# Optimization experiments

Hardware: AMD Instinct MI355X
Metric: run time of the kernel (lower is better)

The kernel has to match this reference:

```python
import jax, jax.numpy as jnp
import numpy as np

EPS = 1e-5
K = 20
THRESH = 0.5

def _bn_relu(x, g, b, m, v):
    # eval-mode BatchNorm1d followed by ReLU
    return jax.nn.relu(g * (x - m) * jax.lax.rsqrt(v + EPS) + b)

def setup_inputs() -> dict:
    key = jax.random.key(0)
    ks = jax.random.split(key, 16)
    T, C, CI, E, NC = 16384, 256, 8, 5, 13
    B, N = 2, T // 2
    inp = {
        "f_sem": jax.random.normal(ks[0], (T, C), jnp.float32),
        "f_ins": jax.random.normal(ks[1], (T, CI), jnp.float32),
        # equal-size, sorted batch assignment (2 clouds of 8192 points)
        "batch": jnp.repeat(jnp.arange(B, dtype=jnp.int64), N),
        # semantic_adaptation_fc: Linear(C,C) + BN + ReLU
        "W_sem": jax.random.normal(ks[2], (C, C), jnp.float32) * (1.0 / np.sqrt(C)),
        "b_sem": jnp.zeros((C,), jnp.float32),
        "g_sem": jnp.ones((C,), jnp.float32),
        "beta_sem": jnp.zeros((C,), jnp.float32),
        "m_sem": jax.random.normal(ks[3], (C,), jnp.float32) * 0.1,
        "v_sem": jax.random.uniform(ks[4], (C,), jnp.float32, 0.5, 1.5),
        # inst_fc: Linear(8,C) + BN + ReLU
        "W_ins": jax.random.normal(ks[5], (CI, C), jnp.float32) * (1.0 / np.sqrt(CI)),
        "b_ins": jnp.zeros((C,), jnp.float32),
        "g_ins": jnp.ones((C,), jnp.float32),
        "beta_ins": jnp.zeros((C,), jnp.float32),
        "m_ins": jax.random.normal(ks[6], (C,), jnp.float32) * 0.1,
        "v_ins": jax.random.uniform(ks[7], (C,), jnp.float32, 0.5, 1.5),
        # instance_embedding_fc: plain Linear(C,E)
        "W_emb": jax.random.normal(ks[8], (C, E), jnp.float32) * (1.0 / np.sqrt(C)),
        "b_emb": jnp.zeros((E,), jnp.float32),
        # classifier_fc: plain Linear(C,NC)
        "W_cls": jax.random.normal(ks[9], (C, NC), jnp.float32) * (1.0 / np.sqrt(C)),
        "b_cls": jnp.zeros((NC,), jnp.float32),
    }
    return inp

def _instance_fusion(e_ins, f_sem, batch):
    # assumes sorted batch with equal-size segments (enforced by setup_inputs)
    T, C = f_sem.shape
    B = int(batch[-1]) + 1
    N = T // B
    e = e_ins.reshape(B, N, -1)
    f = f_sem.reshape(B, N, C)
    # squared Euclidean pairwise distances per cloud: [B, N, N]
    sq = jnp.sum(e * e, axis=-1)
    d2 = sq[:, :, None] + sq[:, None, :] - 2.0 * jnp.einsum("bnd,bmd->bnm", e, e)
    d2 = jnp.maximum(d2, 0.0)
    neg_vals, idx = jax.lax.top_k(-d2, K)          # k smallest distances, [B,N,K]
    within = (-neg_vals) <= THRESH * THRESH        # distance <= threshold
    self_idx = jnp.broadcast_to(jnp.arange(N)[None, :, None], idx.shape)
    col = jnp.where(within, idx, self_idx)         # fall back to self outside threshold
    neigh = jax.vmap(lambda fb, cb: fb[cb])(f, col)  # [B,N,K,C]
    return jnp.max(neigh, axis=2).reshape(T, C)      # scatter-max == max over neighbors

def reference(f_sem, f_ins, batch,
              W_sem, b_sem, g_sem, beta_sem, m_sem, v_sem,
              W_ins, b_ins, g_ins, beta_ins, m_ins, v_ins,
              W_emb, b_emb, W_cls, b_cls):
    f_sem_prime = _bn_relu(f_sem @ W_sem + b_sem, g_sem, beta_sem, m_sem, v_sem)
    f_ins_h = _bn_relu(f_ins @ W_ins + b_ins, g_ins, beta_ins, m_ins, v_ins)
    f_sins = f_ins_h + f_sem_prime
    e_ins = f_sins @ W_emb + b_emb
    f_isem = _instance_fusion(e_ins, f_sem, batch)
    p_sem = f_isem @ W_cls + b_cls
    return (p_sem, e_ins)
```

## Files before the change

### kernel.cpp

```cpp
#include <hip/hip_runtime.h>
#include <math.h>

#define T 16384
#define C 256
#define CI 8
#define EDIM 5
#define NC 13
#define NPTS 8192
#define KNN 20
#define CAP 256
#define FR 32
#define FRPB 8

typedef float f4v __attribute__((ext_vector_type(4)));
typedef _Float16 h8 __attribute__((ext_vector_type(8)));
typedef _Float16 h4v __attribute__((ext_vector_type(4)));

__global__ __launch_bounds__(256) void cvt_kernel(
    const float* __restrict__ f_sem, _Float16* __restrict__ fsem_h)
{
    const size_t i = (size_t)(blockIdx.x * 256 + threadIdx.x) * 8;
    const float4 a = *(const float4*)(f_sem + i);
    const float4 b = *(const float4*)(f_sem + i + 4);
    h8 h;
    h[0] = (_Float16)a.x; h[1] = (_Float16)a.y;
    h[2] = (_Float16)a.z; h[3] = (_Float16)a.w;
    h[4] = (_Float16)b.x; h[5] = (_Float16)b.y;
    h[6] = (_Float16)b.z; h[7] = (_Float16)b.w;
    *(h8*)(fsem_h + i) = h;
}

__global__ __launch_bounds__(256) void front_kernel(
    const float* __restrict__ f_sem, const float* __restrict__ f_ins,
    const float* __restrict__ W_sem, const float* __restrict__ b_sem,
    const float* __restrict__ g_sem, const float* __restrict__ beta_sem,
    const float* __restrict__ m_sem, const float* __restrict__ v_sem,
    const float* __restrict__ W_ins, const float* __restrict__ b_ins,
    const float* __restrict__ g_ins, const float* __restrict__ beta_ins,
    const float* __restrict__ m_ins, const float* __restrict__ v_ins,
    const float* __restrict__ W_emb, const float* __restrict__ b_emb,
    float* __restrict__ eA, double* __restrict__ eD,
    float* __restrict__ out_e)
{
    __shared__ __align__(16) _Float16 sAh[FR][264];
    __shared__ __align__(16) _Float16 sAl[FR][264];
    __shared__ float bnA1[C], bnB1[C], bnA2[C], bnB2[C];
    __shared__ float weL[C][EDIM];
    __shared__ float lfi[FR][CI];
    __shared__ float sP[4][FR][EDIM];

    const int tid = threadIdx.x;
    const int rowBase = blockIdx.x * FR;

    #pragma unroll
    for (int i = 0; i < 8; i++) {
        const int idx = tid + 256 * i;
        const int g = idx * 4;
        const int row = g >> 8, k = g & 255;
        const float4 v = *(const float4*)(f_sem + (size_t)rowBase * C + g);
        const float vv[4] = {v.x, v.y, v.z, v.w};
        #pragma unroll
        for (int q = 0; q < 4; q++) {
            const _Float16 h = (_Float16)vv[q];
            sAh[row][k + q] = h;
            sAl[row][k + q] = (_Float16)(vv[q] - (float)h);
        }
    }
    {
        const int c = tid;
        const float rs1 = 1.0f / sqrtf(v_sem[c] + 1e-5f);
        const float A1 = g_sem[c] * rs1;
        bnA1[c] = A1;
        bnB1[c] = A1 * (b_sem[c] - m_sem[c]) + beta_sem[c];
        const float rs2 = 1.0f / sqrtf(v_ins[c] + 1e-5f);
        const float A2 = g_ins[c] * rs2;
        bnA2[c] = A2;
        bnB2[c] = A2 * (b_ins[c] - m_ins[c]) + beta_ins[c];
        #pragma unroll
        for (int j = 0; j < EDIM; j++) weL[c][j] = W_emb[c * EDIM + j];
    }
    if (tid < FR * CI) lfi[tid >> 3][tid & 7] = f_ins[rowBase * CI + tid];
    __syncthreads();

    const int w = tid >> 6, lane = tid & 63;
    const int r16 = lane & 15, kq = lane >> 4;
    const int n0 = 64 * w;

    f4v acc[2][4];
    #pragma unroll
    for (int mi = 0; mi < 2; mi++)
        #pragma unroll
        for (int ni = 0; ni < 4; ni++) acc[mi][ni] = (f4v){0.f, 0.f, 0.f, 0.f};

    for (int kt = 0; kt < 8; kt++) {
        const int koff = 32 * kt + 8 * kq;
        const h8 ah0 = *(const h8*)&sAh[r16][koff];
        const h8 ah1 = *(const h8*)&sAh[r16 + 16][koff];
        const h8 al0 = *(const h8*)&sAl[r16][koff];
        const h8 al1 = *(const h8*)&sAl[r16 + 16][koff];
        #pragma unroll
        for (int ni = 0; ni < 4; ni++) {
            const float* wp = W_sem + (size_t)koff * C + (n0 + 16 * ni + r16);
            float wf[8];
            #pragma unroll
            for (int j = 0; j < 8; j++) wf[j] = wp[(size_t)j * C];
            h8 bh, bl;
            #pragma unroll
            for (int j = 0; j < 8; j++) {
                const _Float16 h = (_Float16)wf[j];
                bh[j] = h;
                bl[j] = (_Float16)(wf[j] - (float)h);
            }
            acc[0][ni] = __builtin_amdgcn_mfma_f32_16x16x32_f16(ah0, bh, acc[0][ni], 0, 0, 0);
            acc[1][ni] = __builtin_amdgcn_mfma_f32_16x16x32_f16(ah1, bh, acc[1][ni], 0, 0, 0);
            acc[0][ni] = __builtin_amdgcn_mfma_f32_16x16x32_f16(al0, bh, acc[0][ni], 0, 0, 0);
            acc[1][ni] = __builtin_amdgcn_mfma_f32_16x16x32_f16(al1, bh, acc[1][ni], 0, 0, 0);
            acc[0][ni] = __builtin_amdgcn_mfma_f32_16x16x32_f16(ah0, bl, acc[0][ni], 0, 0, 0);
            acc[1][ni] = __builtin_amdgcn_mfma_f32_16x16x32_f16(ah1, bl, acc[1][ni], 0, 0, 0);
        }
    }

    f4v prow, pcol;
    {
        const f4v z = {0.f, 0.f, 0.f, 0.f};
        h8 ra, rb, ca, cb;
        #pragma unroll
        for (int j = 0; j < 8; j++) {
            ra[j] = (_Float16)(float)r16;
            rb[j] = (_Float16)((kq == 0 && j == 0) ? 1.0f : 0.0f);
            ca[j] = rb[j];
            cb[j] = ra[j];
        }
        prow = __builtin_amdgcn_mfma_f32_16x16x32_f16(ra, rb, z, 0, 0, 0);
        pcol = __builtin_amdgcn_mfma_f32_16x16x32_f16(ca, cb, z, 0, 0, 0);
    }
    const int colm = (int)pcol[0];
    int rloc[4];
    #pragma unroll
    for (int r = 0; r < 4; r++) rloc[r] = (int)prow[r];

    float p[2][4][EDIM];
    #pragma unroll
    for (int mi = 0; mi < 2; mi++)
        #pragma unroll
        for (int r = 0; r < 4; r++)
            #pragma unroll
            for (int j = 0; j < EDIM; j++) p[mi][r][j] = 0.f;

    #pragma unroll
    for (int ni = 0; ni < 4; ni++) {
        const int c = n0 + 16 * ni + colm;
        const float A1 = bnA1[c], B1 = bnB1[c];
        const float A2 = bnA2[c], B2 = bnB2[c];
        float wi[CI], we[EDIM];
        #pragma unroll
        for (int k = 0; k < CI; k++) wi[k] = W_ins[k * C + c];
        #pragma unroll
        for (int j = 0; j < EDIM; j++) we[j] = weL[c][j];
        #pragma unroll
        for (int mi = 0; mi < 2; mi++)
            #pragma unroll
            for (int r = 0; r < 4; r++) {
                const int row = 16 * mi + rloc[r];
                float x2 = 0.f;
                #pragma unroll
                for (int k = 0; k < CI; k++) x2 = fmaf(lfi[row][k], wi[k], x2);
                const float h1 = fmaxf(fmaf(A1, acc[mi][ni][r], B1), 0.f);
                const float h2 = fmaxf(fmaf(A2, x2, B2), 0.f);
                const float s = h1 + h2;
                #pragma unroll
                for (int j = 0; j < EDIM; j++) p[mi][r][j] = fmaf(s, we[j], p[mi][r][j]);
            }
    }

    #pragma unroll
    for (int off = 1; off < 16; off <<= 1)
        #pragma unroll
        for (int mi = 0; mi < 2; mi++)
            #pragma unroll
            for (int r = 0; r < 4; r++)
                #pragma unroll
                for (int j = 0; j < EDIM; j++)
                    p[mi][r][j] += __shfl_xor(p[mi][r][j], off);

    if (r16 == 0) {
        #pragma unroll
        for (int mi = 0; mi < 2; mi++)
            #pragma unroll
            for (int r = 0; r < 4; r++)
                #pragma unroll
                for (int j = 0; j < EDIM; j++)
                    sP[w][16 * mi + rloc[r]][j] = p[mi][r][j];
    }
    __syncthreads();

    if (tid < FR) {
        const int row = rowBase + tid;
        double sq = 0.0;
        #pragma unroll
        for (int j = 0; j < EDIM; j++) {
            const float s = ((sP[0][tid][j] + sP[1][tid][j]) +
                             (sP[2][tid][j] + sP[3][tid][j])) + b_emb[j];
            const double ed = (double)s;
            eD[(size_t)row * 8 + j] = ed;
            sq = fma(ed, ed, sq);
            eA[(size_t)row * 8 + j] = s;
            out_e[(size_t)row * EDIM + j] = s;
        }
        eD[(size_t)row * 8 + 5] = sq;
        eA[(size_t)row * 8 + 5] = (float)sq;
        eA[(size_t)row * 8 + 6] = 0.f;
        eA[(size_t)row * 8 + 7] = 0.f;
    }
}

__device__ __attribute__((noinline)) float4 rescan_topk(
    const float* __restrict__ eA, const float* __restrict__ f_sem,
    const float* __restrict__ reRow, int cbase, int lane)
{
    float re0 = reRow[0], re1 = reRow[1], re2 = reRow[2];
    float re3 = reRow[3], re4 = reRow[4], sqF = reRow[5];
    float4 mx = make_float4(-3.4e38f, -3.4e38f, -3.4e38f, -3.4e38f);
    long long last = -1;
    for (int sel = 0; sel < KNN; sel++) {
        long long best = 0x7fffffffffffffffLL;
        for (int cb = 0; cb < NPTS; cb += 64) {
            const int j = cbase + cb + lane;
            const float4 ea = *(const float4*)(eA + (size_t)j * 8);
            const float2 eb = *(const float2*)(eA + (size_t)j * 8 + 4);
            float dot = re0 * ea.x;
            dot = fmaf(re1, ea.y, dot); dot = fmaf(re2, ea.z, dot);
            dot = fmaf(re3, ea.w, dot); dot = fmaf(re4, eb.x, dot);
            const float d2 = fmaxf((sqF + eb.y) - 2.f * dot, 0.f);
            long long key = (((long long)__float_as_uint(d2)) << 32)
                            | (unsigned int)(cb + lane);
            if (key <= last) key = 0x7fffffffffffffffLL;
            if (key < best) best = key;
        }
        #pragma unroll
        for (int off = 32; off; off >>= 1) {
            const long long o = __shfl_xor(best, off);
            if (o < best) best = o;
        }
        last = best;
        const int idx = (int)(best & 0xffffffffLL);
        const float4 fv = *(const float4*)(f_sem + (size_t)(cbase + idx) * C + lane * 4);
        mx.x = fmaxf(mx.x, fv.x); mx.y = fmaxf(mx.y, fv.y);
        mx.z = fmaxf(mx.z, fv.z); mx.w = fmaxf(mx.w, fv.w);
    }
    return mx;
}

template <bool H16>
__global__ __launch_bounds__(256) void knn_kernel(
    const float* __restrict__ eA, const double* __restrict__ eD,
    const float* __restrict__ f_sem, const _Float16* __restrict__ fsem_h,
    const float* __restrict__ W_cls, const float* __restrict__ b_cls,
    float* __restrict__ out_p)
{
    __shared__ float rA[FRPB][8];
    __shared__ double rD[FRPB][6];
    __shared__ unsigned short cidx[FRPB][CAP];
    __shared__ unsigned long long kP[FRPB][CAP];
    __shared__ int cntS[FRPB];
    __shared__ unsigned short memL[FRPB][24];
    __shared__ int nlS[FRPB];

    const int tid = threadIdx.x;
    const int rowBase = blockIdx.x * FRPB;

    if (tid < FRPB * 8) rA[tid >> 3][tid & 7] = eA[(rowBase + (tid >> 3)) * 8 + (tid & 7)];
    if (tid < FRPB * 6) rD[tid / 6][tid % 6] = eD[(rowBase + tid / 6) * 8 + tid % 6];
    if (tid < FRPB) cntS[tid] = 0;
    __syncthreads();

    const int wave = tid >> 6, lane = tid & 63;
    const int cbase = (rowBase >= NPTS) ? NPTS : 0;

    {
        float re[FRPB][5], thrb[FRPB];
        #pragma unroll
        for (int r = 0; r < FRPB; r++) {
            #pragma unroll
            for (int q = 0; q < 5; q++) re[r][q] = rA[r][q];
            thrb[r] = (rA[r][5] - 0.251f) * 0.5f;
        }

        const int cstart = wave * (NPTS / 4);
        for (int cb = cstart; cb < cstart + NPTS / 4; cb += 128) {
            const int j0 = cbase + cb + lane;
            const float4 ea0 = *(const float4*)(eA + (size_t)j0 * 8);
            const float2 eb0 = *(const float2*)(eA + (size_t)j0 * 8 + 4);
            const float4 ea1 = *(const float4*)(eA + (size_t)(j0 + 64) * 8);
            const float2 eb1 = *(const float2*)(eA + (size_t)(j0 + 64) * 8 + 4);
            const float hs0 = 0.5f * eb0.y, hs1 = 0.5f * eb1.y;
            #pragma unroll
            for (int r = 0; r < FRPB; r++) {
                float dot = re[r][0] * ea0.x;
                dot = fmaf(re[r][1], ea0.y, dot); dot = fmaf(re[r][2], ea0.z, dot);
                dot = fmaf(re[r][3], ea0.w, dot); dot = fmaf(re[r][4], eb0.x, dot);
                const bool rec = dot >= (thrb[r] + hs0);
                const unsigned long long m = __ballot(rec);
                if (m) {
                    int base;
                    if (lane == 0) base = atomicAdd(&cntS[r], (int)__popcll(m));
                    base = __shfl(base, 0);
                    const int pre = __builtin_amdgcn_mbcnt_hi(
                        (unsigned int)(m >> 32),
                        __builtin_amdgcn_mbcnt_lo((unsigned int)m, 0u));
                    const int pos = base + pre;
                    if (rec && pos < CAP) cidx[r][pos] = (unsigned short)(cb + lane);
                }
            }
            #pragma unroll
            for (int r = 0; r < FRPB; r++) {
                float dot = re[r][0] * ea1.x;
                dot = fmaf(re[r][1], ea1.y, dot); dot = fmaf(re[r][2], ea1.z, dot);
                dot = fmaf(re[r][3], ea1.w, dot); dot = fmaf(re[r][4], eb1.x, dot);
                const bool rec = dot >= (thrb[r] + hs1);
                const unsigned long long m = __ballot(rec);
                if (m) {
                    int base;
                    if (lane == 0) base = atomicAdd(&cntS[r], (int)__popcll(m));
                    base = __shfl(base, 0);
                    const int pre = __builtin_amdgcn_mbcnt_hi(
                        (unsigned int)(m >> 32),
                        __builtin_amdgcn_mbcnt_lo((unsigned int)m, 0u));
                    const int pos = base + pre;
                    if (rec && pos < CAP) cidx[r][pos] = (unsigned short)(cb + 64 + lane);
                }
            }
        }
    }
    __syncthreads();

    const int lr0 = 2 * wave, lr1 = lr0 + 1;

    #pragma unroll 1
    for (int rr = 0; rr < 2; rr++) {
        const int lr = lr0 + rr;
        const int cnt = cntS[lr];
        const double* rd = rD[lr];

        if (cnt <= CAP) {
            unsigned long long mykp[4];
            int myid[4], mpos[4];
            bool mem[4];
            #pragma unroll
            for (int q = 0; q < 4; q++) {
                const int i = lane + 64 * q;
                mykp[q] = ~0ull; myid[q] = -1; mem[q] = false;
                if (i < cnt) {
                    const int id = (int)cidx[lr][i];
                    const double* ep = eD + (size_t)(cbase + id) * 8;
                    double dotd = 0.0;
                    #pragma unroll
                    for (int qq = 0; qq < 5; qq++) dotd = fma(rd[qq], ep[qq], dotd);
                    const double d2 = fmax((rd[5] + ep[5]) - 2.0 * dotd, 0.0);
                    if (d2 <= 0.25) {
                        mem[q] = true;
                        const unsigned int k32 = __float_as_uint((float)d2);
                        mykp[q] = (((unsigned long long)k32) << 16) | (unsigned int)id;
                        myid[q] = id;
                    }
                }
            }
            int base = 0;
            #pragma unroll
            for (int q = 0; q < 4; q++) {
                const unsigned long long b = __ballot(mem[q]);
                if (mem[q]) {
                    const int pos = base + (int)__builtin_amdgcn_mbcnt_hi(
                        (unsigned int)(b >> 32),
                        __builtin_amdgcn_mbcnt_lo((unsigned int)b, 0u));
                    mpos[q] = pos;
                    kP[lr][pos] = mykp[q];
                }
                base += (int)__popcll(b);
            }
            const int m = base;

            if (m <= KNN) {
                #pragma unroll
                for (int q = 0; q < 4; q++)
                    if (mem[q]) memL[lr][mpos[q]] = (unsigned short)myid[q];
                if (lane == 0) nlS[lr] = m;
            } else {
                int rank[4] = {0, 0, 0, 0};
                for (int j = 0; j < m; j++) {
                    const unsigned long long kj = kP[lr][j];
                    #pragma unroll
                    for (int q = 0; q < 4; q++) rank[q] += (kj < mykp[q]) ? 1 : 0;
                }
                int sbase = 0;
                #pragma unroll
                for (int q = 0; q < 4; q++) {
                    const bool sel = mem[q] && (rank[q] < KNN);
                    const unsigned long long b = __ballot(sel);
                    if (sel) {
                        const int pos = sbase + (int)__builtin_amdgcn_mbcnt_hi(
                            (unsigned int)(b >> 32),
                            __builtin_amdgcn_mbcnt_lo((unsigned int)b, 0u));
                        memL[lr][pos] = (unsigned short)myid[q];
                    }
                    sbase += (int)__popcll(b);
                }
                if (lane == 0) nlS[lr] = sbase;
            }
        } else {
            if (lane == 0) { memL[lr][0] = 0; nlS[lr] = -1; }
        }
    }

    const int s0 = nlS[lr0], s1 = nlS[lr1];
    const bool fb0 = (s0 < 0), fb1 = (s1 < 0);
    const int n0 = fb0 ? 1 : s0, n1 = fb1 ? 1 : s1;
    float4 mx0 = make_float4(-3.4e38f, -3.4e38f, -3.4e38f, -3.4e38f);
    float4 mx1 = mx0;
    const int nmax = (n0 > n1) ? n0 : n1;

    if (H16) {
        for (int k = 0; k < nmax; k += 8) {
            int a[8], c[8];
            #pragma unroll
            for (int i = 0; i < 8; i++) {
                a[i] = (int)memL[lr0][(k + i < n0) ? k + i : n0 - 1];
                c[i] = (int)memL[lr1][(k + i < n1) ? k + i : n1 - 1];
            }
            h4v fa[8], fc[8];
            #pragma unroll
            for (int i = 0; i < 8; i++) {
                fa[i] = *(const h4v*)(fsem_h + (size_t)(cbase + a[i]) * C + lane * 4);
                fc[i] = *(const h4v*)(fsem_h + (size_t)(cbase + c[i]) * C + lane * 4);
            }
            #pragma unroll
            for (int i = 0; i < 8; i++) {
                mx0.x = fmaxf(mx0.x, (float)fa[i][0]);
                mx0.y = fmaxf(mx0.y, (float)fa[i][1]);
                mx0.z = fmaxf(mx0.z, (float)fa[i][2]);
                mx0.w = fmaxf(mx0.w, (float)fa[i][3]);
                mx1.x = fmaxf(mx1.x, (float)fc[i][0]);
                mx1.y = fmaxf(mx1.y, (float)fc[i][1]);
                mx1.z = fmaxf(mx1.z, (float)fc[i][2]);
                mx1.w = fmaxf(mx1.w, (float)fc[i][3]);
            }
        }
    } else {
        for (int k = 0; k < nmax; k += 4) {
            const int a0 = (int)memL[lr0][(k     < n0) ? k     : n0 - 1];
            const int a1 = (int)memL[lr0][(k + 1 < n0) ? k + 1 : n0 - 1];
            const int a2 = (int)memL[lr0][(k + 2 < n0) ? k + 2 : n0 - 1];
            const int a3 = (int)memL[lr0][(k + 3 < n0) ? k + 3 : n0 - 1];
            const int c0 = (int)memL[lr1][(k     < n1) ? k     : n1 - 1];
            const int c1 = (int)memL[lr1][(k + 1 < n1) ? k + 1 : n1 - 1];
            const int c2 = (int)memL[lr1][(k + 2 < n1) ? k + 2 : n1 - 1];
            const int c3 = (int)memL[lr1][(k + 3 < n1) ? k + 3 : n1 - 1];
            const float4 f0 = *(const float4*)(f_sem + (size_t)(cbase + a0) * C + lane * 4);
            const float4 f1 = *(const float4*)(f_sem + (size_t)(cbase + a1) * C + lane * 4);
            const float4 f2 = *(const float4*)(f_sem + (size_t)(cbase + a2) * C + lane * 4);
            const float4 f3 = *(const float4*)(f_sem + (size_t)(cbase + a3) * C + lane * 4);
            const float4 g0 = *(const float4*)(f_sem + (size_t)(cbase + c0) * C + lane * 4);
            const float4 g1 = *(const float4*)(f_sem + (size_t)(cbase + c1) * C + lane * 4);
            const float4 g2 = *(const float4*)(f_sem + (size_t)(cbase + c2) * C + lane * 4);
            const float4 g3 = *(const float4*)(f_sem + (size_t)(cbase + c3) * C + lane * 4);
            mx0.x = fmaxf(fmaxf(fmaxf(mx0.x, f0.x), fmaxf(f1.x, f2.x)), f3.x);
            mx0.y = fmaxf(fmaxf(fmaxf(mx0.y, f0.y), fmaxf(f1.y, f2.y)), f3.y);
            mx0.z = fmaxf(fmaxf(fmaxf(mx0.z, f0.z), fmaxf(f1.z, f2.z)), f3.z);
            mx0.w = fmaxf(fmaxf(fmaxf(mx0.w, f0.w), fmaxf(f1.w, f2.w)), f3.w);
            mx1.x = fmaxf(fmaxf(fmaxf(mx1.x, g0.x), fmaxf(g1.x, g2.x)), g3.x);
            mx1.y = fmaxf(fmaxf(fmaxf(mx1.y, g0.y), fmaxf(g1.y, g2.y)), g3.y);
            mx1.z = fmaxf(fmaxf(fmaxf(mx1.z, g0.z), fmaxf(g1.z, g2.z)), g3.z);
            mx1.w = fmaxf(fmaxf(fmaxf(mx1.w, g0.w), fmaxf(g1.w, g2.w)), g3.w);
        }
    }
    if (fb0) mx0 = rescan_topk(eA, f_sem, rA[lr0], cbase, lane);
    if (fb1) mx1 = rescan_topk(eA, f_sem, rA[lr1], cbase, lane);

    #pragma unroll 1
    for (int rr = 0; rr < 2; rr++) {
        const float4 mx = rr ? mx1 : mx0;
        float p[NC];
        #pragma unroll
        for (int k = 0; k < NC; k++) p[k] = 0.f;
        const float* w0 = W_cls + (4 * lane + 0) * NC;
        const float* w1 = W_cls + (4 * lane + 1) * NC;
        const float* w2 = W_cls + (4 * lane + 2) * NC;
        const float* w3 = W_cls + (4 * lane + 3) * NC;
        #pragma unroll
        for (int k = 0; k < NC; k++)
            p[k] = fmaf(mx.x, w0[k], fmaf(mx.y, w1[k], fmaf(mx.z, w2[k], fmaf(mx.w, w3[k], p[k]))));
        #pragma unroll
        for (int off = 32; off; off >>= 1)
            #pragma unroll
            for (int k = 0; k < NC; k++) p[k] += __shfl_xor(p[k], off);
        if (lane == 0) {
            const int row = rowBase + lr0 + rr;
            #pragma unroll
            for (int k = 0; k < NC; k++) out_p[row * NC + k] = p[k] + b_cls[k];
        }
    }
}

extern "C" void kernel_launch(void* const* d_in, const int* in_sizes, int n_in,
                              void* d_out, int out_size, void* d_ws, size_t ws_size,
                              hipStream_t stream) {
    (void)in_sizes; (void)n_in; (void)out_size;
    const float* f_sem    = (const float*)d_in[0];
    const float* f_ins    = (const float*)d_in[1];
    const float* W_sem    = (const float*)d_in[3];
    const float* b_sem    = (const float*)d_in[4];
    const float* g_sem    = (const float*)d_in[5];
    const float* beta_sem = (const float*)d_in[6];
    const float* m_sem    = (const float*)d_in[7];
    const float* v_sem    = (const float*)d_in[8];
    const float* W_ins    = (const float*)d_in[9];
    const float* b_ins    = (const float*)d_in[10];
    const float* g_ins    = (const float*)d_in[11];
    const float* beta_ins = (const float*)d_in[12];
    const float* m_ins    = (const float*)d_in[13];
    const float* v_ins    = (const float*)d_in[14];
    const float* W_emb    = (const float*)d_in[15];
    const float* b_emb    = (const float*)d_in[16];
    const float* W_cls    = (const float*)d_in[17];
    const float* b_cls    = (const float*)d_in[18];
    float* outp = (float*)d_out;

    char* ws = (char*)d_ws;
    float*    eA     = (float*)ws;
    double*   eD     = (double*)(ws + (size_t)T * 8 * 4);
    _Float16* fsem_h = (_Float16*)(ws + (size_t)T * 8 * 12);

    const size_t need_h16 = (size_t)T * 8 * 12 + (size_t)T * C * 2;
    const bool h16 = (ws_size >= need_h16);

    if (h16)
        cvt_kernel<<<T * C / (256 * 8), 256, 0, stream>>>(f_sem, fsem_h);
    front_kernel<<<T / FR, 256, 0, stream>>>(
        f_sem, f_ins, W_sem, b_sem, g_sem, beta_sem, m_sem, v_sem,
        W_ins, b_ins, g_ins, beta_ins, m_ins, v_ins, W_emb, b_emb,
        eA, eD, outp + T * NC);
    if (h16)
        knn_kernel<true><<<T / FRPB, 256, 0, stream>>>(
            eA, eD, f_sem, fsem_h, W_cls, b_cls, outp);
    else
        knn_kernel<false><<<T / FRPB, 256, 0, stream>>>(
            eA, eD, f_sem, (const _Float16*)nullptr, W_cls, b_cls, outp);
}
```

Before: 172.7 us.

## Fold fp16 conversion into front kernel blocks and simplify candidate append

The separate f32-to-fp16 conversion kernel is removed. Its work now runs in extra grid-stride blocks appended to the front kernel's grid, which saves a launch and lets the conversion overlap with the front MLP blocks. Separately, the KNN candidate-recording loop replaces the wave-level ballot/mbcnt aggregated append with a per-lane LDS atomicAdd when the threshold test passes. That removes the ballot and shuffle overhead, at the cost of more LDS atomic contention when many lanes qualify.

```diff
diff --git a/kernel.cpp b/kernel.cpp
--- a/kernel.cpp
+++ b/kernel.cpp
@@ -11,24 +11,11 @@
 #define CAP 256
 #define FR 32
 #define FRPB 8
+#define NCVT 256
 
 typedef float f4v __attribute__((ext_vector_type(4)));
 typedef _Float16 h8 __attribute__((ext_vector_type(8)));
 typedef _Float16 h4v __attribute__((ext_vector_type(4)));
-
-__global__ __launch_bounds__(256) void cvt_kernel(
-    const float* __restrict__ f_sem, _Float16* __restrict__ fsem_h)
-{
-    const size_t i = (size_t)(blockIdx.x * 256 + threadIdx.x) * 8;
-    const float4 a = *(const float4*)(f_sem + i);
-    const float4 b = *(const float4*)(f_sem + i + 4);
-    h8 h;
-    h[0] = (_Float16)a.x; h[1] = (_Float16)a.y;
-    h[2] = (_Float16)a.z; h[3] = (_Float16)a.w;
-    h[4] = (_Float16)b.x; h[5] = (_Float16)b.y;
-    h[6] = (_Float16)b.z; h[7] = (_Float16)b.w;
-    *(h8*)(fsem_h + i) = h;
-}
 
 __global__ __launch_bounds__(256) void front_kernel(
     const float* __restrict__ f_sem, const float* __restrict__ f_ins,
@@ -40,8 +27,26 @@
     const float* __restrict__ m_ins, const float* __restrict__ v_ins,
     const float* __restrict__ W_emb, const float* __restrict__ b_emb,
     float* __restrict__ eA, double* __restrict__ eD,
-    float* __restrict__ out_e)
+    float* __restrict__ out_e, _Float16* __restrict__ fsem_h)
 {
+    const int nFront = T / FR;
+    if (blockIdx.x >= nFront) {
+        const size_t total = (size_t)T * C;
+        const size_t stride = (size_t)NCVT * 256 * 8;
+        size_t i = ((size_t)(blockIdx.x - nFront) * 256 + threadIdx.x) * 8;
+        for (; i < total; i += stride) {
+            const float4 a = *(const float4*)(f_sem + i);
+            const float4 b = *(const float4*)(f_sem + i + 4);
+            h8 h;
+            h[0] = (_Float16)a.x; h[1] = (_Float16)a.y;
+            h[2] = (_Float16)a.z; h[3] = (_Float16)a.w;
+            h[4] = (_Float16)b.x; h[5] = (_Float16)b.y;
+            h[6] = (_Float16)b.z; h[7] = (_Float16)b.w;
+            *(h8*)(fsem_h + i) = h;
+        }
+        return;
+    }
+
     __shared__ __align__(16) _Float16 sAh[FR][264];
     __shared__ __align__(16) _Float16 sAl[FR][264];
     __shared__ float bnA1[C], bnB1[C], bnA2[C], bnB2[C];
@@ -299,17 +304,9 @@
                 float dot = re[r][0] * ea0.x;
                 dot = fmaf(re[r][1], ea0.y, dot); dot = fmaf(re[r][2], ea0.z, dot);
                 dot = fmaf(re[r][3], ea0.w, dot); dot = fmaf(re[r][4], eb0.x, dot);
-                const bool rec = dot >= (thrb[r] + hs0);
-                const unsigned long long m = __ballot(rec);
-                if (m) {
-                    int base;
-                    if (lane == 0) base = atomicAdd(&cntS[r], (int)__popcll(m));
-                    base = __shfl(base, 0);
-                    const int pre = __builtin_amdgcn_mbcnt_hi(
-                        (unsigned int)(m >> 32),
-                        __builtin_amdgcn_mbcnt_lo((unsigned int)m, 0u));
-                    const int pos = base + pre;
-                    if (rec && pos < CAP) cidx[r][pos] = (unsigned short)(cb + lane);
+                if (dot >= (thrb[r] + hs0)) {
+                    const int pos = atomicAdd(&cntS[r], 1);
+                    if (pos < CAP) cidx[r][pos] = (unsigned short)(cb + lane);
                 }
             }
             #pragma unroll
@@ -317,17 +314,9 @@
                 float dot = re[r][0] * ea1.x;
                 dot = fmaf(re[r][1], ea1.y, dot); dot = fmaf(re[r][2], ea1.z, dot);
                 dot = fmaf(re[r][3], ea1.w, dot); dot = fmaf(re[r][4], eb1.x, dot);
-                const bool rec = dot >= (thrb[r] + hs1);
-                const unsigned long long m = __ballot(rec);
-                if (m) {
-                    int base;
-                    if (lane == 0) base = atomicAdd(&cntS[r], (int)__popcll(m));
-                    base = __shfl(base, 0);
-                    const int pre = __builtin_amdgcn_mbcnt_hi(
-                        (unsigned int)(m >> 32),
-                        __builtin_amdgcn_mbcnt_lo((unsigned int)m, 0u));
-                    const int pos = base + pre;
-                    if (rec && pos < CAP) cidx[r][pos] = (unsigned short)(cb + 64 + lane);
+                if (dot >= (thrb[r] + hs1)) {
+                    const int pos = atomicAdd(&cntS[r], 1);
+                    if (pos < CAP) cidx[r][pos] = (unsigned short)(cb + 64 + lane);
                 }
             }
         }
@@ -533,12 +522,11 @@
     const size_t need_h16 = (size_t)T * 8 * 12 + (size_t)T * C * 2;
     const bool h16 = (ws_size >= need_h16);
 
-    if (h16)
-        cvt_kernel<<<T * C / (256 * 8), 256, 0, stream>>>(f_sem, fsem_h);
-    front_kernel<<<T / FR, 256, 0, stream>>>(
+    const int nFront = T / FR;
+    front_kernel<<<h16 ? nFront + NCVT : nFront, 256, 0, stream>>>(
         f_sem, f_ins, W_sem, b_sem, g_sem, beta_sem, m_sem, v_sem,
         W_ins, b_ins, g_ins, beta_ins, m_ins, v_ins, W_emb, b_emb,
-        eA, eD, outp + T * NC);
+        eA, eD, outp + T * NC, h16 ? fsem_h : (_Float16*)nullptr);
     if (h16)
         knn_kernel<true><<<T / FRPB, 256, 0, stream>>>(
             eA, eD, f_sem, fsem_h, W_cls, b_cls, outp);
```

Measured after the change: 167.9 us. 1.03x faster.
